# Kernel optimization log

Hardware: AMD Instinct MI355X
Metric: run time of the kernel (lower is better)

Reference implementation:

```python
import jax, jax.numpy as jnp
import numpy as np

B, S_IMG, S_TXT, P, D, HEADS, HD = 1, 2048, 512, 4, 3072, 24, 128


def rmsnorm(x, weight=None, eps=1e-6):
    var = jnp.mean(jnp.square(x), axis=-1, keepdims=True)
    y = x * jax.lax.rsqrt(var + eps)
    return y * weight if weight is not None else y


def apply_rope(x, cos, sin):
    # x: [B,H,S,Dh]; cos/sin: [S,Dh]; interleaved real/imag rotation (diffusers use_real_unbind_dim=-1)
    xr = x.reshape(*x.shape[:-1], -1, 2)
    rot = jnp.stack([-xr[..., 1], xr[..., 0]], axis=-1).reshape(x.shape)
    return x * cos[None, None] + rot * sin[None, None]


def sdpa(q, k, v):
    scores = jnp.einsum('bhqd,bhkd->bhqk', q, k) / jnp.sqrt(jnp.asarray(q.shape[-1], q.dtype))
    return jnp.einsum('bhqk,bhkd->bhqd', jax.nn.softmax(scores, axis=-1), v)


def heads_split(x):
    # [B,S,D] -> [B,H,S,Dh]
    return x.reshape(x.shape[0], x.shape[1], HEADS, HD).transpose(0, 2, 1, 3)


def heads_merge(x):
    # [B,H,S,Dh] -> [B,S,D]
    return x.transpose(0, 2, 1, 3).reshape(x.shape[0], x.shape[2], HEADS * HD)


def setup_inputs() -> dict:
    key = jax.random.key(0)
    ks = jax.random.split(key, 32)
    init = lambda k, shape: (jax.random.normal(k, shape, dtype=jnp.float32) * 0.02)
    inp = {
        'hidden_states': jax.random.normal(ks[0], (B, S_IMG, D), dtype=jnp.float32),
        'encoder_hidden_states': jax.random.normal(ks[1], (B, S_TXT, D), dtype=jnp.float32),
        'ip_encoder_hidden_states': jax.random.normal(ks[2], (B, P, D), dtype=jnp.float32),
        'layer_scale': jax.random.uniform(ks[3], (B,), dtype=jnp.float32),
        'Wq': init(ks[4], (D, D)), 'bq': jnp.zeros((D,), jnp.float32),
        'Wk': init(ks[5], (D, D)), 'bk': jnp.zeros((D,), jnp.float32),
        'Wv': init(ks[6], (D, D)), 'bv': jnp.zeros((D,), jnp.float32),
        'norm_q_w': jnp.ones((HD,), jnp.float32),
        'norm_k_w': jnp.ones((HD,), jnp.float32),
        'Waq': init(ks[7], (D, D)), 'baq': jnp.zeros((D,), jnp.float32),
        'Wak': init(ks[8], (D, D)), 'bak': jnp.zeros((D,), jnp.float32),
        'Wav': init(ks[9], (D, D)), 'bav': jnp.zeros((D,), jnp.float32),
        'norm_aq_w': jnp.ones((HD,), jnp.float32),
        'norm_ak_w': jnp.ones((HD,), jnp.float32),
        'Wk_ip': init(ks[10], (D, D)),
        'Wv_ip': init(ks[11], (D, D)),
        'Wo': init(ks[12], (D, D)), 'bo': jnp.zeros((D,), jnp.float32),
        'Wao': init(ks[13], (D, D)), 'bao': jnp.zeros((D,), jnp.float32),
    }
    # rotary cos/sin over the joint (text+image) sequence, interleaved freqs per diffusers FLUX
    pos = jnp.arange(S_TXT + S_IMG, dtype=jnp.float32)
    inv_freq = 1.0 / (10000.0 ** (jnp.arange(0, HD, 2, dtype=jnp.float32) / HD))
    angles = pos[:, None] * inv_freq[None, :]            # [S, HD/2]
    angles = jnp.repeat(angles, 2, axis=-1)              # [S, HD]
    inp['cos'] = jnp.cos(angles)
    inp['sin'] = jnp.sin(angles)
    return inp


IP_SCALE = 1.0  # self.scale


def reference(hidden_states, encoder_hidden_states, ip_encoder_hidden_states, cos, sin,
              layer_scale, Wq, bq, Wk, bk, Wv, bv, norm_q_w, norm_k_w,
              Waq, baq, Wak, bak, Wav, bav, norm_aq_w, norm_ak_w,
              Wk_ip, Wv_ip, Wo, bo, Wao, bao):
    # image-stream projections
    q = heads_split(hidden_states @ Wq.T + bq)
    k = heads_split(hidden_states @ Wk.T + bk)
    v = heads_split(hidden_states @ Wv.T + bv)
    q = rmsnorm(q, norm_q_w, 1e-6)
    k = rmsnorm(k, norm_k_w, 1e-6)

    # IP-adapter cross-attention (queries = image tokens, kv = IP tokens)
    ip_k = rmsnorm(heads_split(ip_encoder_hidden_states @ Wk_ip.T), None, 1e-5)
    ip_v = heads_split(ip_encoder_hidden_states @ Wv_ip.T)
    ip_out = heads_merge(sdpa(q, ip_k, ip_v))            # [B, S_img, D]

    # text (encoder) stream projections, prepended to joint sequence
    eq = rmsnorm(heads_split(encoder_hidden_states @ Waq.T + baq), norm_aq_w, 1e-6)
    ek = rmsnorm(heads_split(encoder_hidden_states @ Wak.T + bak), norm_ak_w, 1e-6)
    ev = heads_split(encoder_hidden_states @ Wav.T + bav)
    q = jnp.concatenate([eq, q], axis=2)
    k = jnp.concatenate([ek, k], axis=2)
    v = jnp.concatenate([ev, v], axis=2)

    q = apply_rope(q, cos, sin)
    k = apply_rope(k, cos, sin)

    out = heads_merge(sdpa(q, k, v))                     # [B, S_txt+S_img, D]
    n_txt = encoder_hidden_states.shape[1]
    enc_out, img_out = out[:, :n_txt], out[:, n_txt:]

    ls = layer_scale.reshape(-1, 1, 1)
    img_out = img_out + IP_SCALE * ls * ip_out
    img_out = img_out @ Wo.T + bo
    enc_out = enc_out @ Wao.T + bao
    return (img_out, enc_out)
```

## Files before the change

kernel.cpp:

```cpp
#include <hip/hip_runtime.h>

typedef _Float16 half_t;
typedef _Float16 half2v __attribute__((ext_vector_type(2)));
typedef _Float16 half4v __attribute__((ext_vector_type(4)));
typedef _Float16 half8v __attribute__((ext_vector_type(8)));
typedef float    float4v __attribute__((ext_vector_type(4)));
typedef short    short8v __attribute__((ext_vector_type(8)));

#define S_IMG 2048
#define S_TXT 512
#define S_TOT 2560
#define NH    24
#define HD    128
#define DM    3072
#define WSZC  9437184L
#define HSZC  6291456L
#define ESZC  1572864L

__device__ __forceinline__ void gload16(const void* g, void* l) {
  __builtin_amdgcn_global_load_lds(
      (const __attribute__((address_space(1))) unsigned int*)g,
      (__attribute__((address_space(3))) unsigned int*)l, 16, 0, 0);
}

__device__ __forceinline__ void cvt8span(const float* s, half_t* d, long i) {
  float4v v0 = *(const float4v*)(s + i);
  float4v v1 = *(const float4v*)(s + i + 4);
  half8v h;
  h[0] = (half_t)v0[0]; h[1] = (half_t)v0[1]; h[2] = (half_t)v0[2]; h[3] = (half_t)v0[3];
  h[4] = (half_t)v1[0]; h[5] = (half_t)v1[1]; h[6] = (half_t)v1[2]; h[7] = (half_t)v1[3];
  *(half8v*)(d + i) = h;
}

__global__ void cvt_act_kernel(const float* __restrict__ hs, const float* __restrict__ enc,
                               half_t* __restrict__ d) {
  const long TOT = HSZC + ESZC;
  long i = ((long)blockIdx.x * 256 + threadIdx.x) * 8;
  long stride = (long)gridDim.x * 256 * 8;
  for (; i < TOT; i += stride) {
    const float* s = i < HSZC ? hs + i : enc + (i - HSZC);
    cvt8span(s, d + i, 0);
  }
}

__global__ void cvt3_kernel(const float* __restrict__ s0, const float* __restrict__ s1,
                            const float* __restrict__ s2,
                            half_t* __restrict__ d0, half_t* __restrict__ d1,
                            half_t* __restrict__ d2, int n) {
  const float* s = blockIdx.y == 0 ? s0 : (blockIdx.y == 1 ? s1 : s2);
  half_t* d = blockIdx.y == 0 ? d0 : (blockIdx.y == 1 ? d1 : d2);
  long i = ((long)blockIdx.x * 256 + threadIdx.x) * 8;
  long stride = (long)gridDim.x * 256 * 8;
  for (; i < n; i += stride) cvt8span(s, d, i);
}

__global__ void cvt8_kernel(const float* w0, const float* w1, const float* w2,
                            const float* w3, const float* w4, const float* w5,
                            const float* hs, const float* enc,
                            half_t* __restrict__ W6, half_t* __restrict__ hs_h) {
  int y = blockIdx.y;
  const float* s;
  half_t* d;
  long n;
  if (y < 6) {
    s = y == 0 ? w0 : y == 1 ? w1 : y == 2 ? w2 : y == 3 ? w3 : y == 4 ? w4 : w5;
    d = W6 + (long)y * WSZC;
    n = WSZC;
  } else if (y == 6) { s = hs; d = hs_h; n = HSZC; }
  else               { s = enc; d = hs_h + HSZC; n = ESZC; }
  long i = ((long)blockIdx.x * 256 + threadIdx.x) * 8;
  long stride = (long)gridDim.x * 256 * 8;
  for (; i < n; i += stride) cvt8span(s, d, i);
}

template <typename OUT>
__device__ __forceinline__ void gemm_tile(half_t* As, half_t* Bs,
                                          const half_t* __restrict__ A,
                                          const half_t* __restrict__ Bt,
                                          const float* __restrict__ bias,
                                          OUT* __restrict__ C, int bm, int bn) {
  const int K = DM, N = DM;
  const int tid = threadIdx.x, wid = tid >> 6, l = tid & 63;
  const int wm = (wid >> 1) * 64, wn = (wid & 1) * 64;
  const int l15 = l & 15, l4 = l >> 4;
  float4v acc[4][4] = {};

  const int scol = ((l & 3) ^ ((l >> 3) & 3)) * 8;
  const half_t* ga = A + (long)(bm + wid * 32 + (l >> 2)) * K + scol;
  const half_t* gb = Bt + (long)(bn + wid * 32 + (l >> 2)) * K + scol;
  const long rowstep = 16l * K;

#define GSTAGE(T, SEL)                                                        \
  {                                                                           \
    char* a_d = (char*)As + (SEL) * 8192 + wid * 2048;                        \
    char* b_d = (char*)Bs + (SEL) * 8192 + wid * 2048;                        \
    int k0 = (T) * 32;                                                        \
    gload16(ga + k0, a_d);                                                    \
    gload16(ga + rowstep + k0, a_d + 1024);                                   \
    gload16(gb + k0, b_d);                                                    \
    gload16(gb + rowstep + k0, b_d + 1024);                                   \
  }

  GSTAGE(0, 0);

  const int NT = K / 32;
  const int cofs = (l4 * 16) ^ (((l15 >> 1) & 3) << 4);
  int sel = 0;
  for (int t = 0; t < NT; t++) {
    asm volatile("s_waitcnt vmcnt(0)" ::: "memory");
    __builtin_amdgcn_s_barrier();
    __builtin_amdgcn_sched_barrier(0);
    if (t + 1 < NT) GSTAGE(t + 1, sel ^ 1);
    __builtin_amdgcn_sched_barrier(0);
    const char* AsB = (const char*)As + sel * 8192;
    const char* BsB = (const char*)Bs + sel * 8192;
    half8v af[4], bf[4];
#pragma unroll
    for (int i = 0; i < 4; i++)
      af[i] = *(const half8v*)(AsB + (wm + i * 16 + l15) * 64 + cofs);
#pragma unroll
    for (int j = 0; j < 4; j++)
      bf[j] = *(const half8v*)(BsB + (wn + j * 16 + l15) * 64 + cofs);
    __builtin_amdgcn_s_setprio(1);
#pragma unroll
    for (int i = 0; i < 4; i++)
#pragma unroll
      for (int j = 0; j < 4; j++)
        acc[i][j] = __builtin_amdgcn_mfma_f32_16x16x32_f16(af[i], bf[j], acc[i][j], 0, 0, 0);
    __builtin_amdgcn_s_setprio(0);
    sel ^= 1;
  }
#undef GSTAGE
#pragma unroll
  for (int i = 0; i < 4; i++)
#pragma unroll
    for (int j = 0; j < 4; j++) {
      int row = bm + wm + i * 16 + l4 * 4;
      int col = bn + wn + j * 16 + l15;
      float bv = bias ? bias[col] : 0.0f;
#pragma unroll
      for (int r = 0; r < 4; r++) {
        float v = acc[i][j][r] + bv;
        C[(long)(row + r) * N + col] = (OUT)v;
      }
    }
}

__global__ __launch_bounds__(256) void gemm_qkv_kernel(
    const half_t* __restrict__ hs_h, const half_t* __restrict__ enc_h,
    const half_t* __restrict__ W6,
    const float* bq, const float* bk, const float* bv,
    const float* baq, const float* bak, const float* bav,
    half_t* q_raw, half_t* k_raw, half_t* v_raw,
    half_t* eq_r, half_t* ek_r, half_t* ev_r) {
  __shared__ half_t As[2 * 4096];
  __shared__ half_t Bs[2 * 4096];
  int b = blockIdx.x;
  int wg = (b & 7) * 180 + (b >> 3);
  const half_t* A;
  const half_t* Bt;
  const float* bias;
  half_t* C;
  int bm, bn;
  if (wg < 1152) {
    int col = wg / 16, row = wg % 16;
    int sel = col / 24;
    A = hs_h; bm = row * 128; bn = (col % 24) * 128;
    Bt = W6 + (long)sel * WSZC;
    bias = sel == 0 ? bq : (sel == 1 ? bk : bv);
    C = sel == 0 ? q_raw : (sel == 1 ? k_raw : v_raw);
  } else {
    int w2 = wg - 1152;
    int col = w2 / 4, row = w2 % 4;
    int sel = col / 24;
    A = enc_h; bm = row * 128; bn = (col % 24) * 128;
    Bt = W6 + (long)(3 + sel) * WSZC;
    bias = sel == 0 ? baq : (sel == 1 ? bak : bav);
    C = sel == 0 ? eq_r : (sel == 1 ? ek_r : ev_r);
  }
  gemm_tile<half_t>(As, Bs, A, Bt, bias, C, bm, bn);
}

template <int NROW>
__global__ __launch_bounds__(256) void gemm3_kernel(const half_t* __restrict__ A,
                                                    const half_t* __restrict__ W0,
                                                    const half_t* __restrict__ W1,
                                                    const half_t* __restrict__ W2,
                                                    const float* b0, const float* b1, const float* b2,
                                                    half_t* O0, half_t* O1, half_t* O2) {
  __shared__ half_t As[2 * 4096];
  __shared__ half_t Bs[2 * 4096];
  int b = blockIdx.x;
  int q = (72 * NROW) >> 3;
  int wg = (b & 7) * q + (b >> 3);
  int col = wg / NROW, row = wg % NROW;
  int sel = col / 24;
  const half_t* Bt = sel == 0 ? W0 : (sel == 1 ? W1 : W2);
  const float* bias = sel == 0 ? b0 : (sel == 1 ? b1 : b2);
  half_t* C = sel == 0 ? O0 : (sel == 1 ? O1 : O2);
  gemm_tile<half_t>(As, Bs, A, Bt, bias, C, row * 128, (col % 24) * 128);
}

__global__ __launch_bounds__(256) void gemm_out_kernel(const half_t* __restrict__ ocomb,
                                                       const half_t* __restrict__ Wo_h,
                                                       const half_t* __restrict__ Wao_h,
                                                       const float* bo, const float* bao,
                                                       float* out_img, float* out_enc) {
  __shared__ half_t As[2 * 4096];
  __shared__ half_t Bs[2 * 4096];
  int b = blockIdx.x;
  int wg = (b & 7) * 60 + (b >> 3);
  int col = wg / 20, r = wg % 20;
  bool enc = r >= 16;
  const half_t* A = enc ? ocomb : ocomb + (long)S_TXT * DM;
  int bm = (enc ? (r - 16) : r) * 128;
  gemm_tile<float>(As, Bs, A, enc ? Wao_h : Wo_h, enc ? bao : bo,
                   enc ? out_enc : out_img, bm, col * 128);
}

__global__ __launch_bounds__(256) void ip_proj_kernel(const float* __restrict__ x,
                                                      const float* __restrict__ Wk_ip,
                                                      const float* __restrict__ Wv_ip,
                                                      float* __restrict__ outk,
                                                      float* __restrict__ outv) {
  const float* W = blockIdx.y ? Wv_ip : Wk_ip;
  float* out = blockIdx.y ? outv : outk;
  int n = blockIdx.x * 4 + (threadIdx.x >> 6);
  int l = threadIdx.x & 63;
  const float* wr = W + (long)n * DM;
  float acc[4] = {0.f, 0.f, 0.f, 0.f};
  for (int k = l * 4; k < DM; k += 256) {
    float4v wv = *(const float4v*)(wr + k);
#pragma unroll
    for (int p = 0; p < 4; p++) {
      float4v xv = *(const float4v*)(x + p * DM + k);
      acc[p] += wv[0] * xv[0] + wv[1] * xv[1] + wv[2] * xv[2] + wv[3] * xv[3];
    }
  }
#pragma unroll
  for (int off = 32; off; off >>= 1)
#pragma unroll
    for (int p = 0; p < 4; p++) acc[p] += __shfl_xor(acc[p], off, 64);
  if (l == 0)
#pragma unroll
    for (int p = 0; p < 4; p++) out[p * DM + n] = acc[p];
}

__global__ void ip_norm_kernel(const float* __restrict__ kr, const float* __restrict__ vr,
                               half_t* __restrict__ kh, half_t* __restrict__ vh) {
  int t = blockIdx.x;
  int l = threadIdx.x;
  int d = l * 2;
  if (t < 96) {
    int base = (t / 24) * DM + (t % 24) * HD;
    float x0 = kr[base + d], x1 = kr[base + d + 1];
    float ss = x0 * x0 + x1 * x1;
#pragma unroll
    for (int off = 32; off; off >>= 1) ss += __shfl_xor(ss, off, 64);
    float r = rsqrtf(ss * (1.0f / HD) + 1e-5f);
    kh[base + d] = (half_t)(x0 * r);
    kh[base + d + 1] = (half_t)(x1 * r);
  } else {
    int t2 = t - 96;
    int base = (t2 / 24) * DM + (t2 % 24) * HD;
    vh[base + d] = (half_t)vr[base + d];
    vh[base + d + 1] = (half_t)vr[base + d + 1];
  }
}

__global__ __launch_bounds__(256) void prep_vtrans_kernel(
    const half_t* __restrict__ qraw, const half_t* __restrict__ kraw,
    const half_t* __restrict__ eq, const half_t* __restrict__ ek,
    const half_t* __restrict__ ev, const half_t* __restrict__ vraw,
    const float* __restrict__ nqw, const float* __restrict__ nkw,
    const float* __restrict__ naqw, const float* __restrict__ nakw,
    const float* __restrict__ cosb, const float* __restrict__ sinb,
    half_t* __restrict__ qcat, half_t* __restrict__ kcat, half_t* __restrict__ qnr,
    half_t* __restrict__ vcatT) {
  __shared__ half_t T[64][136];
  if (blockIdx.x < 15360) {
    int task = blockIdx.x * 4 + (threadIdx.x >> 6);
    int l = threadIdx.x & 63;
    int s = task / NH, h = task - (task / NH) * NH;
    int d = l * 2;
    const half_t *qs, *ks;
    const float *wq, *wk;
    if (s < S_TXT) {
      long base = (long)s * DM + h * HD;
      qs = eq + base; ks = ek + base;
      wq = naqw; wk = nakw;
    } else {
      long base = (long)(s - S_TXT) * DM + h * HD;
      qs = qraw + base; ks = kraw + base;
      wq = nqw; wk = nkw;
    }
    half2v qv = *(const half2v*)(qs + d);
    half2v kv = *(const half2v*)(ks + d);
    float q0 = (float)qv[0], q1 = (float)qv[1];
    float k0 = (float)kv[0], k1 = (float)kv[1];
    float ssq = q0 * q0 + q1 * q1;
    float ssk = k0 * k0 + k1 * k1;
#pragma unroll
    for (int off = 32; off; off >>= 1) {
      ssq += __shfl_xor(ssq, off, 64);
      ssk += __shfl_xor(ssk, off, 64);
    }
    float rq = rsqrtf(ssq * (1.0f / HD) + 1e-6f);
    float rk = rsqrtf(ssk * (1.0f / HD) + 1e-6f);
    float qn0 = q0 * rq * wq[d], qn1 = q1 * rq * wq[d + 1];
    float kn0 = k0 * rk * wk[d], kn1 = k1 * rk * wk[d + 1];
    if (s >= S_TXT) {
      half2v o; o[0] = (half_t)qn0; o[1] = (half_t)qn1;
      *(half2v*)(qnr + ((long)h * S_IMG + (s - S_TXT)) * HD + d) = o;
    }
    float c0 = cosb[s * HD + d], c1 = cosb[s * HD + d + 1];
    float s0 = sinb[s * HD + d], s1 = sinb[s * HD + d + 1];
    float qo0 = qn0 * c0 - qn1 * s0, qo1 = qn1 * c1 + qn0 * s1;
    float ko0 = kn0 * c0 - kn1 * s0, ko1 = kn1 * c1 + kn0 * s1;
    long ci = ((long)h * S_TOT + s) * HD + d;
    half2v oq; oq[0] = (half_t)qo0; oq[1] = (half_t)qo1;
    half2v ok; ok[0] = (half_t)ko0; ok[1] = (half_t)ko1;
    *(half2v*)(qcat + ci) = oq;
    *(half2v*)(kcat + ci) = ok;
  } else {
    int b2 = blockIdx.x - 15360;
    int h = b2 / 40, sb = (b2 % 40) * 64;
    int t = threadIdx.x;
#pragma unroll
    for (int i = 0; i < 4; i++) {
      int c = t + i * 256;
      int row = c >> 4, col = (c & 15) * 8;
      int s = sb + row;
      const half_t* src = (s < S_TXT) ? ev + (long)s * DM + h * HD + col
                                      : vraw + (long)(s - S_TXT) * DM + h * HD + col;
      *(half8v*)&T[row][col] = *(const half8v*)src;
    }
    __syncthreads();
#pragma unroll
    for (int i = 0; i < 4; i++) {
      int c = t + i * 256;
      int d = c >> 3, sc = (c & 7) * 8;
      half8v v;
#pragma unroll
      for (int j = 0; j < 8; j++) v[j] = T[sc + j][d];
      int base = (sc & 32) | ((sc & 8) << 1) | ((sc & 16) >> 2);
      half_t* dst = vcatT + ((long)h * HD + d) * S_TOT + sb;
      half4v q0; q0[0] = v[0]; q0[1] = v[1]; q0[2] = v[2]; q0[3] = v[3];
      half4v q1; q1[0] = v[4]; q1[1] = v[5]; q1[2] = v[6]; q1[7 - 7] = q1[0]; q1[0] = v[4]; q1[1] = v[5]; q1[2] = v[6]; q1[3] = v[7];
      *(half4v*)(dst + base) = q0;
      *(half4v*)(dst + base + 8) = q1;
    }
  }
}

__global__ __launch_bounds__(256) void ip_attn_kernel(const half_t* __restrict__ qnr,
                                                      const half_t* __restrict__ kh,
                                                      const half_t* __restrict__ vh,
                                                      half_t* __restrict__ ipout) {
  int tid = threadIdx.x;
  int task = blockIdx.x * 16 + (tid >> 4);
  int l16 = tid & 15;
  int h = task >> 11;
  int s = task & 2047;
  int d = l16 * 8;
  half8v qv = *(const half8v*)(qnr + ((long)h * S_IMG + s) * HD + d);
  float sc[4];
#pragma unroll
  for (int p = 0; p < 4; p++) {
    half8v kv = *(const half8v*)(kh + p * DM + h * HD + d);
    float a = 0.f;
#pragma unroll
    for (int j = 0; j < 8; j++) a += (float)qv[j] * (float)kv[j];
    sc[p] = a;
  }
#pragma unroll
  for (int off = 8; off; off >>= 1)
#pragma unroll
    for (int p = 0; p < 4; p++) sc[p] += __shfl_xor(sc[p], off, 16);
  float m = fmaxf(fmaxf(sc[0], sc[1]), fmaxf(sc[2], sc[3]));
  float e[4], sum = 0.f;
#pragma unroll
  for (int p = 0; p < 4; p++) { e[p] = __expf((sc[p] - m) * 0.088388347648318447f); sum += e[p]; }
  float inv = 1.0f / sum;
  float o[8] = {};
#pragma unroll
  for (int p = 0; p < 4; p++) {
    half8v vv = *(const half8v*)(vh + p * DM + h * HD + d);
#pragma unroll
    for (int j = 0; j < 8; j++) o[j] += e[p] * (float)vv[j];
  }
  half8v ov;
#pragma unroll
  for (int j = 0; j < 8; j++) ov[j] = (half_t)(o[j] * inv);
  *(half8v*)(ipout + (long)s * DM + h * HD + d) = ov;
}

__global__ __launch_bounds__(256, 2) void flash_kernel(const half_t* __restrict__ qcat,
                                                       const half_t* __restrict__ kcat,
                                                       const half_t* __restrict__ vcatT,
                                                       const half_t* __restrict__ ipout,
                                                       const float* __restrict__ lsp,
                                                       half_t* __restrict__ ocomb,
                                                       const float* __restrict__ WoF,
                                                       const float* __restrict__ WaoF,
                                                       half_t* __restrict__ w0d,
                                                       half_t* __restrict__ w1d) {
  __shared__ half_t Ks[2 * 64 * 128];
  __shared__ half_t Vs[2 * 128 * 64];
  if (blockIdx.x >= 480) {
    int cb = blockIdx.x - 480;
    long i = ((long)cb * 256 + threadIdx.x) * 8;
    long stride = (long)(gridDim.x - 480) * 256 * 8;
    for (; i < 2 * WSZC; i += stride) {
      if (i < WSZC) cvt8span(WoF, w0d, i);
      else          cvt8span(WaoF, w1d, i - WSZC);
    }
    return;
  }
  int b = blockIdx.x;
  int wg = (b & 7) * 60 + (b >> 3);
  const int h = wg / 20, qb = wg % 20;
  const int tid = threadIdx.x, wid = tid >> 6, l = tid & 63;
  const int l15 = l & 15, l4 = l >> 4;
  const float CEXP = 0.12754137969983614f;

  half8v qf[2][4];
#pragma unroll
  for (int t = 0; t < 2; t++) {
    int qrow = qb * 128 + wid * 32 + t * 16 + l15;
    const half_t* qp = qcat + ((long)h * S_TOT + qrow) * HD;
#pragma unroll
    for (int kk = 0; kk < 4; kk++) qf[t][kk] = *(const half8v*)(qp + kk * 32 + l4 * 8);
  }
  float4v o[2][8] = {};
  float lsum[2] = {0.f, 0.f};
  const float ls = lsp[0];

  const char* kb = (const char*)(kcat + (long)h * S_TOT * HD);
  const char* vb = (const char*)(vcatT + (long)h * HD * S_TOT);
  int kof[4];
  long vof[4];
#pragma unroll
  for (int c = 0; c < 4; c++) {
    int L = c * 4096 + tid * 16;
    kof[c] = L ^ (((L >> 8) & 7) << 4);
    int vrow = L >> 7;
    vof[c] = (long)vrow * (S_TOT * 2) + ((L & 127) ^ ((vrow & 7) << 4));
  }

#define STAGE(KT, SEL)                                                        \
  {                                                                           \
    char* kd = (char*)Ks + (SEL) * 16384 + wid * 1024;                        \
    char* vd = (char*)Vs + (SEL) * 16384 + wid * 1024;                        \
    _Pragma("unroll") for (int c = 0; c < 4; c++) {                           \
      gload16(kb + (long)(KT) * 256 + kof[c], kd + c * 4096);                 \
      gload16(vb + vof[c] + (KT) * 2, vd + c * 4096);                         \
    }                                                                         \
  }

  STAGE(0, 0);

  const int NT = S_TOT / 64;
  int sel = 0;
  for (int it = 0; it < NT; it++) {
    asm volatile("s_waitcnt vmcnt(0)" ::: "memory");
    __builtin_amdgcn_s_barrier();
    __builtin_amdgcn_sched_barrier(0);
    if (it + 1 < NT) STAGE((it + 1) * 64, sel ^ 1);

    const char* KsB = (const char*)Ks + sel * 16384;
    const char* VsB = (const char*)Vs + sel * 16384;

    float4v s0[4] = {}, s1[4] = {};
    __builtin_amdgcn_s_setprio(1);
#pragma unroll
    for (int nb = 0; nb < 4; nb++) {
      int krow = nb * 16 + l15;
      int rb = krow << 8;
      int sw = (krow & 7) << 4;
#pragma unroll
      for (int kk = 0; kk < 4; kk++) {
        half8v kf = *(const half8v*)(KsB + rb + ((kk * 64 + l4 * 16) ^ sw));
        s0[nb] = __builtin_amdgcn_mfma_f32_16x16x32_f16(kf, qf[0][kk], s0[nb], 0, 0, 0);
        s1[nb] = __builtin_amdgcn_mfma_f32_16x16x32_f16(kf, qf[1][kk], s1[nb], 0, 0, 0);
      }
    }
    __builtin_amdgcn_s_setprio(0);
    half8v pa00, pa01, pa10, pa11;
    {
      float sum0 = 0.f, sum1 = 0.f;
      float e0[4][4], e1[4][4];
#pragma unroll
      for (int nb = 0; nb < 4; nb++)
#pragma unroll
        for (int r = 0; r < 4; r++) {
          float a = exp2f(s0[nb][r] * CEXP - 2.0f);
          float c = exp2f(s1[nb][r] * CEXP - 2.0f);
          e0[nb][r] = a; e1[nb][r] = c;
          sum0 += a; sum1 += c;
        }
      lsum[0] += sum0; lsum[1] += sum1;
#pragma unroll
      for (int r = 0; r < 4; r++) {
        pa00[r] = (half_t)e0[0][r]; pa00[r + 4] = (half_t)e0[1][r];
        pa01[r] = (half_t)e0[2][r]; pa01[r + 4] = (half_t)e0[3][r];
        pa10[r] = (half_t)e1[0][r]; pa10[r + 4] = (half_t)e1[1][r];
        pa11[r] = (half_t)e1[2][r]; pa11[r + 4] = (half_t)e1[3][r];
      }
    }
    __builtin_amdgcn_s_setprio(1);
#pragma unroll
    for (int cb = 0; cb < 8; cb++) {
      int row = cb * 16 + l15;
      int sw = (row & 7) << 4;
      half8v vf0 = *(const half8v*)(VsB + (row << 7) + ((l4 * 16) ^ sw));
      half8v vf1 = *(const half8v*)(VsB + (row << 7) + ((64 + l4 * 16) ^ sw));
      o[0][cb] = __builtin_amdgcn_mfma_f32_16x16x32_f16(pa00, vf0, o[0][cb], 0, 0, 0);
      o[0][cb] = __builtin_amdgcn_mfma_f32_16x16x32_f16(pa01, vf1, o[0][cb], 0, 0, 0);
      o[1][cb] = __builtin_amdgcn_mfma_f32_16x16x32_f16(pa10, vf0, o[1][cb], 0, 0, 0);
      o[1][cb] = __builtin_amdgcn_mfma_f32_16x16x32_f16(pa11, vf1, o[1][cb], 0, 0, 0);
    }
    __builtin_amdgcn_s_setprio(0);
    sel ^= 1;
  }
#undef STAGE
  float lreg[2];
#pragma unroll
  for (int t = 0; t < 2; t++) {
    float s = lsum[t];
    s += __shfl_xor(s, 16, 64);
    s += __shfl_xor(s, 32, 64);
    lreg[t] = s;
  }
#pragma unroll
  for (int t = 0; t < 2; t++) {
    float invq = 1.0f / lreg[t];
#pragma unroll
    for (int r = 0; r < 4; r++) {
      float inv = __shfl(invq, l4 * 4 + r, 64);
      int s = qb * 128 + wid * 32 + t * 16 + l4 * 4 + r;
#pragma unroll
      for (int cb = 0; cb < 8; cb++) {
        int col = h * HD + cb * 16 + l15;
        float val = o[t][cb][r] * inv;
        if (s >= S_TXT) val += ls * (float)ipout[(long)(s - S_TXT) * DM + col];
        ocomb[(long)s * DM + col] = (half_t)val;
      }
    }
  }
}

extern "C" void kernel_launch(void* const* d_in, const int* in_sizes, int n_in,
                              void* d_out, int out_size, void* d_ws, size_t ws_size,
                              hipStream_t stream) {
  (void)in_sizes; (void)n_in; (void)out_size;
  const float* hs    = (const float*)d_in[0];
  const float* enc   = (const float*)d_in[1];
  const float* ipenc = (const float*)d_in[2];
  const float* lsc   = (const float*)d_in[3];
  const float* Wq  = (const float*)d_in[4];  const float* bq  = (const float*)d_in[5];
  const float* Wk  = (const float*)d_in[6];  const float* bk  = (const float*)d_in[7];
  const float* Wv  = (const float*)d_in[8];  const float* bv  = (const float*)d_in[9];
  const float* nqw = (const float*)d_in[10]; const float* nkw = (const float*)d_in[11];
  const float* Waq = (const float*)d_in[12]; const float* baq = (const float*)d_in[13];
  const float* Wak = (const float*)d_in[14]; const float* bak = (const float*)d_in[15];
  const float* Wav = (const float*)d_in[16]; const float* bav = (const float*)d_in[17];
  const float* naqw= (const float*)d_in[18]; const float* nakw= (const float*)d_in[19];
  const float* Wkip= (const float*)d_in[20]; const float* Wvip= (const float*)d_in[21];
  const float* Wo  = (const float*)d_in[22]; const float* bo  = (const float*)d_in[23];
  const float* Wao = (const float*)d_in[24]; const float* bao = (const float*)d_in[25];
  const float* cosb= (const float*)d_in[26]; const float* sinb= (const float*)d_in[27];

  const size_t WSZ = WSZC;
  const size_t HSZ = HSZC;
  const size_t ESZ = ESZC;
  const size_t CSZ = (size_t)NH * S_TOT * HD;
  const size_t REST = HSZ + ESZ + 3 * HSZ + 3 * ESZ + 3 * CSZ;
  const bool big = ws_size >= (6 * WSZ + REST) * sizeof(half_t);
  const int NSLOT = big ? 6 : 3;

  half_t* base = (half_t*)d_ws;
  half_t* Wsl   = base;
  half_t* hs_h  = Wsl + NSLOT * WSZ;
  half_t* enc_h = hs_h + HSZ;
  half_t* qkvr  = enc_h + ESZ;
  half_t* eqkv  = qkvr + 3 * HSZ;
  half_t* qcat  = eqkv + 3 * ESZ;
  half_t* kcat  = qcat + CSZ;
  half_t* vcatT = kcat + CSZ;

  half_t* q_raw = qkvr;
  half_t* k_raw = qkvr + HSZ;
  half_t* v_raw = qkvr + 2 * HSZ;
  half_t* eq_r  = eqkv;
  half_t* ek_r  = eqkv + ESZ;
  half_t* ev_r  = eqkv + 2 * ESZ;
  half_t* qnr   = hs_h;
  half_t* ipout = qkvr;
  half_t* ocomb = qkvr + HSZ;
  float*  ipk_raw = (float*)enc_h;
  float*  ipv_raw = ipk_raw + 4 * DM;
  half_t* ipk_h  = enc_h + 16 * DM;
  half_t* ipv_h  = ipk_h + 4 * DM;

  if (big) {
    cvt8_kernel<<<dim3(1024, 8), 256, 0, stream>>>(Wq, Wk, Wv, Waq, Wak, Wav,
                                                   hs, enc, Wsl, hs_h);
    gemm_qkv_kernel<<<1440, 256, 0, stream>>>(hs_h, enc_h, Wsl,
                                              bq, bk, bv, baq, bak, bav,
                                              q_raw, k_raw, v_raw, eq_r, ek_r, ev_r);
  } else {
    cvt_act_kernel<<<2048, 256, 0, stream>>>(hs, enc, hs_h);
    cvt3_kernel<<<dim3(1024, 3), 256, 0, stream>>>(Wq, Wk, Wv, Wsl, Wsl + WSZ, Wsl + 2 * WSZ, (int)WSZ);
    gemm3_kernel<16><<<1152, 256, 0, stream>>>(hs_h, Wsl, Wsl + WSZ, Wsl + 2 * WSZ,
                                               bq, bk, bv, q_raw, k_raw, v_raw);
    cvt3_kernel<<<dim3(1024, 3), 256, 0, stream>>>(Waq, Wak, Wav, Wsl, Wsl + WSZ, Wsl + 2 * WSZ, (int)WSZ);
    gemm3_kernel<4><<<288, 256, 0, stream>>>(enc_h, Wsl, Wsl + WSZ, Wsl + 2 * WSZ,
                                             baq, bak, bav, eq_r, ek_r, ev_r);
  }

  ip_proj_kernel<<<dim3(768, 2), 256, 0, stream>>>(ipenc, Wkip, Wvip, ipk_raw, ipv_raw);
  ip_norm_kernel<<<192, 64, 0, stream>>>(ipk_raw, ipv_raw, ipk_h, ipv_h);

  prep_vtrans_kernel<<<16320, 256, 0, stream>>>(q_raw, k_raw, eq_r, ek_r, ev_r, v_raw,
                                                nqw, nkw, naqw, nakw, cosb, sinb,
                                                qcat, kcat, qnr, vcatT);

  ip_attn_kernel<<<(NH * S_IMG) / 16, 256, 0, stream>>>(qnr, ipk_h, ipv_h, ipout);

  if (big) {
    flash_kernel<<<480 + 512, 256, 0, stream>>>(qcat, kcat, vcatT, ipout, lsc, ocomb,
                                                Wo, Wao, Wsl, Wsl + WSZ);
  } else {
    flash_kernel<<<480, 256, 0, stream>>>(qcat, kcat, vcatT, ipout, lsc, ocomb,
                                          Wo, Wao, Wsl, Wsl + WSZ);
    cvt3_kernel<<<dim3(1024, 2), 256, 0, stream>>>(Wo, Wao, Wao, Wsl, Wsl + WSZ, Wsl + 2 * WSZ, (int)WSZ);
  }

  float* out_img = (float*)d_out;
  float* out_enc = (float*)d_out + (size_t)S_IMG * DM;
  gemm_out_kernel<<<480, 256, 0, stream>>>(ocomb, Wsl, Wsl + WSZ, bo, bao, out_img, out_enc);
}
```

Baseline: 501.9 us.

## Fold IP-adapter projection and norm into QKV GEMM and prep kernels

Measured after the change: 493.5 us. About the same (-1.7%).

```diff
diff --git a/kernel.cpp b/kernel.cpp
--- a/kernel.cpp
+++ b/kernel.cpp
@@ -73,6 +73,52 @@
   for (; i < n; i += stride) cvt8span(s, d, i);
 }
 
+__device__ __forceinline__ void ip_proj_body(const float* __restrict__ x,
+                                             const float* __restrict__ W,
+                                             float* __restrict__ out, int bx) {
+  int n = bx * 4 + (threadIdx.x >> 6);
+  int l = threadIdx.x & 63;
+  const float* wr = W + (long)n * DM;
+  float acc[4] = {0.f, 0.f, 0.f, 0.f};
+  for (int k = l * 4; k < DM; k += 256) {
+    float4v wv = *(const float4v*)(wr + k);
+#pragma unroll
+    for (int p = 0; p < 4; p++) {
+      float4v xv = *(const float4v*)(x + p * DM + k);
+      acc[p] += wv[0] * xv[0] + wv[1] * xv[1] + wv[2] * xv[2] + wv[3] * xv[3];
+    }
+  }
+#pragma unroll
+  for (int off = 32; off; off >>= 1)
+#pragma unroll
+    for (int p = 0; p < 4; p++) acc[p] += __shfl_xor(acc[p], off, 64);
+  if (l == 0)
+#pragma unroll
+    for (int p = 0; p < 4; p++) out[p * DM + n] = acc[p];
+}
+
+__device__ __forceinline__ void ip_norm_body(const float* __restrict__ kr,
+                                             const float* __restrict__ vr,
+                                             half_t* __restrict__ kh,
+                                             half_t* __restrict__ vh, int t, int l) {
+  int d = l * 2;
+  if (t < 96) {
+    int base = (t / 24) * DM + (t % 24) * HD;
+    float x0 = kr[base + d], x1 = kr[base + d + 1];
+    float ss = x0 * x0 + x1 * x1;
+#pragma unroll
+    for (int off = 32; off; off >>= 1) ss += __shfl_xor(ss, off, 64);
+    float r = rsqrtf(ss * (1.0f / HD) + 1e-5f);
+    kh[base + d] = (half_t)(x0 * r);
+    kh[base + d + 1] = (half_t)(x1 * r);
+  } else {
+    int t2 = t - 96;
+    int base = (t2 / 24) * DM + (t2 % 24) * HD;
+    vh[base + d] = (half_t)vr[base + d];
+    vh[base + d + 1] = (half_t)vr[base + d + 1];
+  }
+}
+
 template <typename OUT>
 __device__ __forceinline__ void gemm_tile(half_t* As, half_t* Bs,
                                           const half_t* __restrict__ A,
@@ -152,10 +198,21 @@
     const float* bq, const float* bk, const float* bv,
     const float* baq, const float* bak, const float* bav,
     half_t* q_raw, half_t* k_raw, half_t* v_raw,
-    half_t* eq_r, half_t* ek_r, half_t* ev_r) {
+    half_t* eq_r, half_t* ek_r, half_t* ev_r,
+    const float* __restrict__ ipenc,
+    const float* __restrict__ Wkip, const float* __restrict__ Wvip,
+    float* __restrict__ ipk_raw, float* __restrict__ ipv_raw) {
   __shared__ half_t As[2 * 4096];
   __shared__ half_t Bs[2 * 4096];
   int b = blockIdx.x;
+  if (b >= 1440) {
+    int b2 = b - 1440;
+    const float* W = b2 >= 768 ? Wvip : Wkip;
+    float* out = b2 >= 768 ? ipv_raw : ipk_raw;
+    int bx = b2 >= 768 ? b2 - 768 : b2;
+    ip_proj_body(ipenc, W, out, bx);
+    return;
+  }
   int wg = (b & 7) * 180 + (b >> 3);
   const half_t* A;
   const half_t* Bt;
@@ -225,47 +282,12 @@
                                                       float* __restrict__ outv) {
   const float* W = blockIdx.y ? Wv_ip : Wk_ip;
   float* out = blockIdx.y ? outv : outk;
-  int n = blockIdx.x * 4 + (threadIdx.x >> 6);
-  int l = threadIdx.x & 63;
-  const float* wr = W + (long)n * DM;
-  float acc[4] = {0.f, 0.f, 0.f, 0.f};
-  for (int k = l * 4; k < DM; k += 256) {
-    float4v wv = *(const float4v*)(wr + k);
-#pragma unroll
-    for (int p = 0; p < 4; p++) {
-      float4v xv = *(const float4v*)(x + p * DM + k);
-      acc[p] += wv[0] * xv[0] + wv[1] * xv[1] + wv[2] * xv[2] + wv[3] * xv[3];
-    }
-  }
-#pragma unroll
-  for (int off = 32; off; off >>= 1)
-#pragma unroll
-    for (int p = 0; p < 4; p++) acc[p] += __shfl_xor(acc[p], off, 64);
-  if (l == 0)
-#pragma unroll
-    for (int p = 0; p < 4; p++) out[p * DM + n] = acc[p];
+  ip_proj_body(x, W, out, blockIdx.x);
 }
 
 __global__ void ip_norm_kernel(const float* __restrict__ kr, const float* __restrict__ vr,
                                half_t* __restrict__ kh, half_t* __restrict__ vh) {
-  int t = blockIdx.x;
-  int l = threadIdx.x;
-  int d = l * 2;
-  if (t < 96) {
-    int base = (t / 24) * DM + (t % 24) * HD;
-    float x0 = kr[base + d], x1 = kr[base + d + 1];
-    float ss = x0 * x0 + x1 * x1;
-#pragma unroll
-    for (int off = 32; off; off >>= 1) ss += __shfl_xor(ss, off, 64);
-    float r = rsqrtf(ss * (1.0f / HD) + 1e-5f);
-    kh[base + d] = (half_t)(x0 * r);
-    kh[base + d + 1] = (half_t)(x1 * r);
-  } else {
-    int t2 = t - 96;
-    int base = (t2 / 24) * DM + (t2 % 24) * HD;
-    vh[base + d] = (half_t)vr[base + d];
-    vh[base + d + 1] = (half_t)vr[base + d + 1];
-  }
+  ip_norm_body(kr, vr, kh, vh, blockIdx.x, threadIdx.x);
 }
 
 __global__ __launch_bounds__(256) void prep_vtrans_kernel(
@@ -276,8 +298,15 @@
     const float* __restrict__ naqw, const float* __restrict__ nakw,
     const float* __restrict__ cosb, const float* __restrict__ sinb,
     half_t* __restrict__ qcat, half_t* __restrict__ kcat, half_t* __restrict__ qnr,
-    half_t* __restrict__ vcatT) {
+    half_t* __restrict__ vcatT,
+    const float* __restrict__ ipk_raw, const float* __restrict__ ipv_raw,
+    half_t* __restrict__ ipk_h, half_t* __restrict__ ipv_h) {
   __shared__ half_t T[64][136];
+  if (blockIdx.x >= 16320) {
+    int task = (blockIdx.x - 16320) * 4 + (threadIdx.x >> 6);
+    ip_norm_body(ipk_raw, ipv_raw, ipk_h, ipv_h, task, threadIdx.x & 63);
+    return;
+  }
   if (blockIdx.x < 15360) {
     int task = blockIdx.x * 4 + (threadIdx.x >> 6);
     int l = threadIdx.x & 63;
@@ -346,7 +375,7 @@
       int base = (sc & 32) | ((sc & 8) << 1) | ((sc & 16) >> 2);
       half_t* dst = vcatT + ((long)h * HD + d) * S_TOT + sb;
       half4v q0; q0[0] = v[0]; q0[1] = v[1]; q0[2] = v[2]; q0[3] = v[3];
-      half4v q1; q1[0] = v[4]; q1[1] = v[5]; q1[2] = v[6]; q1[7 - 7] = q1[0]; q1[0] = v[4]; q1[1] = v[5]; q1[2] = v[6]; q1[3] = v[7];
+      half4v q1; q1[0] = v[4]; q1[1] = v[5]; q1[2] = v[6]; q1[3] = v[7];
       *(half4v*)(dst + base) = q0;
       *(half4v*)(dst + base + 8) = q1;
     }
@@ -575,8 +604,10 @@
   const size_t HSZ = HSZC;
   const size_t ESZ = ESZC;
   const size_t CSZ = (size_t)NH * S_TOT * HD;
+  const size_t IPX = 4 * DM;
+  const size_t EXTRA = 2 * (2 * IPX) + 2 * IPX;
   const size_t REST = HSZ + ESZ + 3 * HSZ + 3 * ESZ + 3 * CSZ;
-  const bool big = ws_size >= (6 * WSZ + REST) * sizeof(half_t);
+  const bool big = ws_size >= (6 * WSZ + REST + EXTRA) * sizeof(half_t);
   const int NSLOT = big ? 6 : 3;
 
   half_t* base = (half_t*)d_ws;
@@ -588,6 +619,7 @@
   half_t* qcat  = eqkv + 3 * ESZ;
   half_t* kcat  = qcat + CSZ;
   half_t* vcatT = kcat + CSZ;
+  half_t* tail  = vcatT + CSZ;
 
   half_t* q_raw = qkvr;
   half_t* k_raw = qkvr + HSZ;
@@ -598,17 +630,34 @@
   half_t* qnr   = hs_h;
   half_t* ipout = qkvr;
   half_t* ocomb = qkvr + HSZ;
-  float*  ipk_raw = (float*)enc_h;
-  float*  ipv_raw = ipk_raw + 4 * DM;
-  half_t* ipk_h  = enc_h + 16 * DM;
-  half_t* ipv_h  = ipk_h + 4 * DM;
+
+  float*  ipk_raw;
+  float*  ipv_raw;
+  half_t* ipk_h;
+  half_t* ipv_h;
+  if (big) {
+    ipk_raw = (float*)tail;
+    ipv_raw = ipk_raw + IPX;
+    ipk_h   = tail + 4 * IPX;
+    ipv_h   = ipk_h + IPX;
+  } else {
+    ipk_raw = (float*)enc_h;
+    ipv_raw = ipk_raw + IPX;
+    ipk_h   = enc_h + 4 * IPX;
+    ipv_h   = ipk_h + IPX;
+  }
 
   if (big) {
     cvt8_kernel<<<dim3(1024, 8), 256, 0, stream>>>(Wq, Wk, Wv, Waq, Wak, Wav,
                                                    hs, enc, Wsl, hs_h);
-    gemm_qkv_kernel<<<1440, 256, 0, stream>>>(hs_h, enc_h, Wsl,
-                                              bq, bk, bv, baq, bak, bav,
-                                              q_raw, k_raw, v_raw, eq_r, ek_r, ev_r);
+    gemm_qkv_kernel<<<1440 + 1536, 256, 0, stream>>>(hs_h, enc_h, Wsl,
+                                                     bq, bk, bv, baq, bak, bav,
+                                                     q_raw, k_raw, v_raw, eq_r, ek_r, ev_r,
+                                                     ipenc, Wkip, Wvip, ipk_raw, ipv_raw);
+    prep_vtrans_kernel<<<16320 + 48, 256, 0, stream>>>(q_raw, k_raw, eq_r, ek_r, ev_r, v_raw,
+                                                       nqw, nkw, naqw, nakw, cosb, sinb,
+                                                       qcat, kcat, qnr, vcatT,
+                                                       ipk_raw, ipv_raw, ipk_h, ipv_h);
   } else {
     cvt_act_kernel<<<2048, 256, 0, stream>>>(hs, enc, hs_h);
     cvt3_kernel<<<dim3(1024, 3), 256, 0, stream>>>(Wq, Wk, Wv, Wsl, Wsl + WSZ, Wsl + 2 * WSZ, (int)WSZ);
@@ -617,14 +666,13 @@
     cvt3_kernel<<<dim3(1024, 3), 256, 0, stream>>>(Waq, Wak, Wav, Wsl, Wsl + WSZ, Wsl + 2 * WSZ, (int)WSZ);
     gemm3_kernel<4><<<288, 256, 0, stream>>>(enc_h, Wsl, Wsl + WSZ, Wsl + 2 * WSZ,
                                              baq, bak, bav, eq_r, ek_r, ev_r);
-  }
-
-  ip_proj_kernel<<<dim3(768, 2), 256, 0, stream>>>(ipenc, Wkip, Wvip, ipk_raw, ipv_raw);
-  ip_norm_kernel<<<192, 64, 0, stream>>>(ipk_raw, ipv_raw, ipk_h, ipv_h);
-
-  prep_vtrans_kernel<<<16320, 256, 0, stream>>>(q_raw, k_raw, eq_r, ek_r, ev_r, v_raw,
-                                                nqw, nkw, naqw, nakw, cosb, sinb,
-                                                qcat, kcat, qnr, vcatT);
+    ip_proj_kernel<<<dim3(768, 2), 256, 0, stream>>>(ipenc, Wkip, Wvip, ipk_raw, ipv_raw);
+    ip_norm_kernel<<<192, 64, 0, stream>>>(ipk_raw, ipv_raw, ipk_h, ipv_h);
+    prep_vtrans_kernel<<<16320, 256, 0, stream>>>(q_raw, k_raw, eq_r, ek_r, ev_r, v_raw,
+                                                  nqw, nkw, naqw, nakw, cosb, sinb,
+                                                  qcat, kcat, qnr, vcatT,
+                                                  ipk_raw, ipv_raw, ipk_h, ipv_h);
+  }
 
   ip_attn_kernel<<<(NH * S_IMG) / 16, 256, 0, stream>>>(qnr, ipk_h, ipv_h, ipout);
 
```
